# Kernel optimization log

Hardware: AMD Instinct MI355X
Metric: run time of the kernel (lower is better)

Reference implementation:

```python
import jax, jax.numpy as jnp
import numpy as np

N_NODES = 100000
N_EDGES = 3200000
D_FEAT = 64
CLAMP = 20.0
POSINF = 1.0e6
NEGINF = -1.0e6


def setup_inputs() -> dict:
    key = jax.random.key(0)
    k1, k2, k3, k4 = jax.random.split(key, 4)
    x = jax.random.normal(k1, (N_NODES, D_FEAT), dtype=jnp.float32)
    edge_src = jax.random.randint(k2, (N_EDGES,), 0, N_NODES, dtype=jnp.int64 if jax.config.jax_enable_x64 else jnp.int32).astype(jnp.int32)
    edge_dst = jax.random.randint(k3, (N_EDGES,), 0, N_NODES, dtype=jnp.int32)
    # symmetric-normalized-adjacency-like positive weights
    edge_w = jax.random.uniform(k4, (N_EDGES,), dtype=jnp.float32)
    t = jnp.zeros((1,), dtype=jnp.float32)
    return {"t": t, "x": x, "edge_src": edge_src, "edge_dst": edge_dst, "edge_w": edge_w}


def reference(t, x, edge_src, edge_dst, edge_w):
    # out = sparse.mm(G, x): out[dst] += w * x[src]  (COO SpMM via segment_sum)
    msgs = edge_w[:, None] * x[edge_src]                 # [E, d]
    out = jax.ops.segment_sum(msgs, edge_dst, num_segments=N_NODES)  # [N, d]
    # numerical_stability epilogue: nan/inf sanitize + clamp
    out = jnp.nan_to_num(out, nan=0.0, posinf=POSINF, neginf=NEGINF)
    out = jnp.clip(out, -CLAMP, CLAMP)
    return out
```

## Files before the change

### kernel.cpp

```cpp
#include <hip/hip_runtime.h>
#include <hip/hip_fp16.h>
#include <math.h>

#define N_NODES 100000
#define N_EDGES 3200000
#define D_FEAT  64
#define CLAMP_V 20.0f

#define BSH 6
#define BSZ 64
#define NB  1563
#define SBNSH 10
#define NSB 98
#define CPAD 32
#define CHUNKP 4096
#define NCHUNK ((N_EDGES + CHUNKP - 1) / CHUNKP)
#define CAPL 2560
#define HISTB 512
#define NSLC 4
#define NBIN 256
#define GRIDSG 1568
#define CPX (GRIDSG / 8)


__global__ __launch_bounds__(256)
void prep_kernel(const float4* __restrict__ xin, ushort4* __restrict__ xh,
                 const int* __restrict__ edst, int* __restrict__ counts,
                 int n4) {
    __shared__ int h[NSB];
    if (blockIdx.x < HISTB) {
        if (threadIdx.x < NSB) h[threadIdx.x] = 0;
        __syncthreads();
        const int4* d4p = (const int4*)edst;
        int total4 = N_EDGES >> 2;
        for (int i = blockIdx.x * blockDim.x + threadIdx.x; i < total4;
             i += HISTB * blockDim.x) {
            int4 d4 = d4p[i];
            atomicAdd(&h[d4.x >> SBNSH], 1);
            atomicAdd(&h[d4.y >> SBNSH], 1);
            atomicAdd(&h[d4.z >> SBNSH], 1);
            atomicAdd(&h[d4.w >> SBNSH], 1);
        }
        __syncthreads();
        if (threadIdx.x < NSB) {
            int v = h[threadIdx.x];
            if (v) atomicAdd(&counts[threadIdx.x * CPAD], v);
        }
    } else {
        int i = (blockIdx.x - HISTB) * blockDim.x + threadIdx.x;
        if (i < n4) {
            float4 v = xin[i];
            ushort4 o;
            o.x = __half_as_ushort(__float2half(v.x));
            o.y = __half_as_ushort(__float2half(v.y));
            o.z = __half_as_ushort(__float2half(v.z));
            o.w = __half_as_ushort(__float2half(v.w));
            xh[i] = o;
        }
    }
}

__global__ void scan_kernel(const int* __restrict__ counts,
                            int* __restrict__ bstartsSB,
                            int* __restrict__ cursors1) {
    __shared__ int wtot[2];
    int t = threadIdx.x;
    int lane = t & 63, wv = t >> 6;
    int c = (t < NSB) ? counts[t * CPAD] : 0;
    int sc = c;
#pragma unroll
    for (int off = 1; off < 64; off <<= 1) {
        int u = __shfl_up(sc, off);
        if (lane >= off) sc += u;
    }
    if (lane == 63) wtot[wv] = sc;
    __syncthreads();
    int base = (wv == 1) ? wtot[0] : 0;
    int excl = base + sc - c;
    if (t < NSB) {
        bstartsSB[t] = excl;
        cursors1[t * CPAD] = excl;
    }
    if (t == 0) bstartsSB[NSB] = N_EDGES;
}

__global__ __launch_bounds__(512)
void pass1_kernel(const int* __restrict__ esrc,
                  const int* __restrict__ edst,
                  const float* __restrict__ ew,
                  int* __restrict__ cursors1,
                  unsigned* __restrict__ rk32,
                  unsigned short* __restrict__ ra16) {
    __shared__ unsigned       spk[CHUNKP];
    __shared__ unsigned short sax[CHUNKP];
    __shared__ unsigned char  binof[CHUNKP];
    __shared__ int h[NSB];
    __shared__ int hstart[NSB];
    __shared__ int lcur[NSB];
    __shared__ int lbase[NSB];
    __shared__ int wtot[2];

    int c0   = blockIdx.x * CHUNKP;
    int cend = min(c0 + CHUNKP, N_EDGES);
    int n    = cend - c0;
    int nv   = n >> 2;
    const int4*   d4p = (const int4*)(edst + c0);
    const int4*   s4p = (const int4*)(esrc + c0);
    const float4* w4p = (const float4*)(ew + c0);
    int t = threadIdx.x;

    if (t < NSB) h[t] = 0;
    __syncthreads();
    for (int i = t; i < nv; i += 512) {
        int4 d4 = d4p[i];
        atomicAdd(&h[d4.x >> SBNSH], 1);
        atomicAdd(&h[d4.y >> SBNSH], 1);
        atomicAdd(&h[d4.z >> SBNSH], 1);
        atomicAdd(&h[d4.w >> SBNSH], 1);
    }
    __syncthreads();
    int c = 0, sc = 0;
    if (t < 128) {
        c = (t < NSB) ? h[t] : 0;
        sc = c;
#pragma unroll
        for (int off = 1; off < 64; off <<= 1) {
            int u = __shfl_up(sc, off);
            if ((t & 63) >= off) sc += u;
        }
        if ((t & 63) == 63) wtot[t >> 6] = sc;
    }
    __syncthreads();
    if (t < NSB) {
        int base = (t >= 64) ? wtot[0] : 0;
        int excl = base + sc - c;
        hstart[t] = excl;
        lcur[t]   = excl;
        lbase[t]  = c ? atomicAdd(&cursors1[t * CPAD], c) : 0;
    }
    __syncthreads();
    for (int i = t; i < nv; i += 512) {
        int4   d4 = d4p[i];
        int4   s4 = s4p[i];
        float4 w4 = w4p[i];
#define PUT(dd, ss, ww)                                                       \
        {                                                                     \
            int bk  = (dd) >> SBNSH;                                          \
            int pos = atomicAdd(&lcur[bk], 1);                                \
            unsigned hw = __half_as_ushort(__float2half(ww));                 \
            spk[pos] = ((hw & 0xFFFEu) << 16) | (unsigned)(ss);               \
            sax[pos] = (unsigned short)((dd) & 1023);                         \
            binof[pos] = (unsigned char)bk;                                   \
        }
        PUT(d4.x, s4.x, w4.x);
        PUT(d4.y, s4.y, w4.y);
        PUT(d4.z, s4.z, w4.z);
        PUT(d4.w, s4.w, w4.w);
#undef PUT
    }
    __syncthreads();
    for (int i = t; i < n; i += 512) {
        int bk = binof[i];
        int o  = lbase[bk] + (i - hstart[bk]);
        rk32[o] = spk[i];
        ra16[o] = sax[i];
    }
}

__global__ __launch_bounds__(512)
void sort_gather_kernel(const __half* __restrict__ xh,
                        const unsigned* __restrict__ rk32,
                        const unsigned short* __restrict__ ra16,
                        const int* __restrict__ bstartsSB,
                        float* __restrict__ out) {
    __shared__ unsigned      sbuf[CAPL];
    __shared__ unsigned      stg[CAPL];
    __shared__ unsigned char sbin[CAPL];
    __shared__ int h[NBIN + 1];
    __shared__ int cur[NBIN];
    __shared__ int wsum4[4];
    __shared__ int mcnt;
    int t    = threadIdx.x;
    int lane = t & 63;
    int wv   = t >> 6;
    int g    = lane >> 4;
    int s    = lane & 15;
    const char* xbase = (const char*)xh + (s << 3);

    int p = blockIdx.x;
    int b = (p & 7) * CPX + (p >> 3);
    if (b >= NB) return;
    int sbid = b >> 4;
    int fk   = b & 15;
    int sbeg = bstartsSB[sbid];
    int send = bstartsSB[sbid + 1];

    if (t <= NBIN) h[t] = 0;
    if (t == 0) mcnt = 0;
    __syncthreads();
    int a0 = sbeg & ~3;
    for (int i0 = a0 + t * 4; i0 < send; i0 += 512 * 4) {
        int4    r4 = *(const int4*)(rk32 + i0);
        ushort4 a4 = *(const ushort4*)(ra16 + i0);
#define FILT(J, RR, AA)                                                       \
        {                                                                     \
            int idx = i0 + (J);                                               \
            if (idx >= sbeg && idx < send && (int)((AA) >> 6) == fk) {        \
                int bin = (int)((((unsigned)(RR) >> 15) & 3u) << 6)           \
                        | (int)((AA) & 63u);                                  \
                int pos = atomicAdd(&mcnt, 1);                                \
                if (pos < CAPL) {                                             \
                    stg[pos]  = (unsigned)(RR);                               \
                    sbin[pos] = (unsigned char)bin;                           \
                    atomicAdd(&h[bin + 1], 1);                                \
                }                                                             \
            }                                                                 \
        }
        FILT(0, r4.x, a4.x);
        FILT(1, r4.y, a4.y);
        FILT(2, r4.z, a4.z);
        FILT(3, r4.w, a4.w);
#undef FILT
    }
    __syncthreads();
    int cnt = mcnt;
    if (cnt > CAPL) cnt = CAPL;
    if (t < NBIN) {
        int sc = h[t + 1];
#pragma unroll
        for (int off = 1; off < 64; off <<= 1) {
            int u = __shfl_up(sc, off);
            if (lane >= off) sc += u;
        }
        if (lane == 63) wsum4[wv] = sc;
        __syncthreads();
        if (t == 0) {
            int r = 0;
#pragma unroll
            for (int j = 0; j < 4; ++j) { int v = wsum4[j]; wsum4[j] = r; r += v; }
        }
        __syncthreads();
        h[t + 1] = sc + wsum4[wv];
    } else {
        __syncthreads();
        __syncthreads();
    }
    __syncthreads();
    if (t < NBIN) cur[t] = h[t];
    __syncthreads();
    for (int e = t; e < cnt; e += 512) {
        sbuf[atomicAdd(&cur[sbin[e]], 1)] = stg[e];
    }
    __syncthreads();

#define GSTEP(EE, K)                                                         \
    {                                                                        \
        unsigned p2 = sbuf[(EE) + g];                                        \
        float wf = __half2float(__ushort_as_half(                            \
                       (unsigned short)((p2 >> 16) & 0xFFFEu)));             \
        const ushort4 xv = *(const ushort4*)(xbase +                         \
                       ((size_t)((p2 & 0x1FFFFu) << 7)));                    \
        ak0[K] = fmaf(__half2float(__ushort_as_half(xv.x)), wf, ak0[K]);     \
        ak1[K] = fmaf(__half2float(__ushort_as_half(xv.y)), wf, ak1[K]);     \
        ak2[K] = fmaf(__half2float(__ushort_as_half(xv.z)), wf, ak2[K]);     \
        ak3[K] = fmaf(__half2float(__ushort_as_half(xv.w)), wf, ak3[K]);     \
    }
#define GSTEPC(EE, S1, K)                                                    \
    {                                                                        \
        int eg = (EE) + g;                                                   \
        unsigned p2 = sbuf[eg < (S1) ? eg : ((S1) - 1)];                     \
        float wf = (eg < (S1)) ? __half2float(__ushort_as_half(              \
                       (unsigned short)((p2 >> 16) & 0xFFFEu))) : 0.0f;      \
        const ushort4 xv = *(const ushort4*)(xbase +                         \
                       ((size_t)((p2 & 0x1FFFFu) << 7)));                    \
        ak0[K] = fmaf(__half2float(__ushort_as_half(xv.x)), wf, ak0[K]);     \
        ak1[K] = fmaf(__half2float(__ushort_as_half(xv.y)), wf, ak1[K]);     \
        ak2[K] = fmaf(__half2float(__ushort_as_half(xv.z)), wf, ak2[K]);     \
        ak3[K] = fmaf(__half2float(__ushort_as_half(xv.w)), wf, ak3[K]);     \
    }

    int node0 = b << BSH;
    float ak0[8], ak1[8], ak2[8], ak3[8];
#pragma unroll
    for (int k = 0; k < 8; ++k) { ak0[k] = 0.f; ak1[k] = 0.f; ak2[k] = 0.f; ak3[k] = 0.f; }
#pragma unroll 1
    for (int blk = 0; blk < NSLC; ++blk) {
#pragma unroll
        for (int k = 0; k < 8; ++k) {
            int seg = (blk << 6) | ((wv << 3) + k);
            int s0 = h[seg];
            int s1 = h[seg + 1];
            int e = s0;
            for (; e + 8 <= s1; e += 8) {
                GSTEP(e, k);
                GSTEP(e + 4, k);
            }
            for (; e + 4 <= s1; e += 4)
                GSTEP(e, k);
            if (e < s1)
                GSTEPC(e, s1, k);
        }
    }
#pragma unroll
    for (int k = 0; k < 8; ++k) {
        float a0 = ak0[k], a1 = ak1[k], a2 = ak2[k], a3 = ak3[k];
        a0 += __shfl_xor(a0, 16); a0 += __shfl_xor(a0, 32);
        a1 += __shfl_xor(a1, 16); a1 += __shfl_xor(a1, 32);
        a2 += __shfl_xor(a2, 16); a2 += __shfl_xor(a2, 32);
        a3 += __shfl_xor(a3, 16); a3 += __shfl_xor(a3, 32);
        if (isnan(a0)) a0 = 0.0f;
        if (isnan(a1)) a1 = 0.0f;
        if (isnan(a2)) a2 = 0.0f;
        if (isnan(a3)) a3 = 0.0f;
        a0 = fminf(fmaxf(a0, -CLAMP_V), CLAMP_V);
        a1 = fminf(fmaxf(a1, -CLAMP_V), CLAMP_V);
        a2 = fminf(fmaxf(a2, -CLAMP_V), CLAMP_V);
        a3 = fminf(fmaxf(a3, -CLAMP_V), CLAMP_V);
        int node = node0 + (wv << 3) + k;
        if (lane < 16 && node < N_NODES)
            *(float4*)(out + ((size_t)node << 6) + (s << 2)) =
                make_float4(a0, a1, a2, a3);
    }
#undef GSTEP
#undef GSTEPC
}

__global__ void zero_kernel(float4* __restrict__ out, int n4) {
    int i = blockIdx.x * blockDim.x + threadIdx.x;
    if (i < n4) out[i] = make_float4(0.f, 0.f, 0.f, 0.f);
}

__global__ void scatter_kernel(const float* __restrict__ x,
                               const int* __restrict__ esrc,
                               const int* __restrict__ edst,
                               const float* __restrict__ ew,
                               float* __restrict__ out) {
    long long tid = (long long)blockIdx.x * blockDim.x + threadIdx.x;
    int edge = (int)(tid >> 4);
    int q    = (int)(tid & 15);
    if (edge >= N_EDGES) return;
    int   s = esrc[edge];
    int   d = edst[edge];
    float w = ew[edge];
    const float4* xrow = (const float4*)(x + (size_t)s * D_FEAT);
    float4 v = xrow[q];
    float* orow = out + (size_t)d * D_FEAT + q * 4;
    atomicAdd(orow + 0, w * v.x);
    atomicAdd(orow + 1, w * v.y);
    atomicAdd(orow + 2, w * v.z);
    atomicAdd(orow + 3, w * v.w);
}

__global__ void epilogue_kernel(float4* __restrict__ out, int n4) {
    int i = blockIdx.x * blockDim.x + threadIdx.x;
    if (i >= n4) return;
    float4 v = out[i];
    float* p = &v.x;
#pragma unroll
    for (int k = 0; k < 4; ++k) {
        float f = p[k];
        if (isnan(f)) f = 0.0f;
        f = fminf(fmaxf(f, -CLAMP_V), CLAMP_V);
        p[k] = f;
    }
    out[i] = v;
}

extern "C" void kernel_launch(void* const* d_in, const int* in_sizes, int n_in,
                              void* d_out, int out_size, void* d_ws, size_t ws_size,
                              hipStream_t stream) {
    const float* x    = (const float*)d_in[1];
    const int*   esrc = (const int*)d_in[2];
    const int*   edst = (const int*)d_in[3];
    const float* ew   = (const float*)d_in[4];
    float*       out  = (float*)d_out;

    size_t meta_ints = (size_t)NSB * CPAD
                     + (NSB + 1)
                     + (size_t)NSB * CPAD;
    meta_ints = (meta_ints + 3) & ~(size_t)3;
    size_t rk_bytes  = (size_t)N_EDGES * sizeof(unsigned);
    size_t ra_bytes  = (size_t)N_EDGES * sizeof(unsigned short);
    size_t xh_bytes  = (size_t)N_NODES * D_FEAT * sizeof(__half);
    size_t need = meta_ints * sizeof(int) + rk_bytes + ra_bytes + xh_bytes;

    if (ws_size >= need) {
        int*      counts    = (int*)d_ws;
        int*      bstartsSB = counts + (size_t)NSB * CPAD;
        int*      cursors1  = bstartsSB + (NSB + 1);
        unsigned* rk32      = (unsigned*)((int*)d_ws + meta_ints);
        unsigned short* ra16 = (unsigned short*)((char*)rk32 + rk_bytes);
        __half*   xh        = (__half*)((char*)ra16 + ra_bytes);

        hipMemsetAsync(counts, 0, (size_t)NSB * CPAD * sizeof(int), stream);
        {
            int n4 = N_NODES * D_FEAT / 4;
            prep_kernel<<<HISTB + (n4 + 255) / 256, 256, 0, stream>>>(
                (const float4*)x, (ushort4*)xh, edst, counts, n4);
        }
        scan_kernel<<<1, 128, 0, stream>>>(counts, bstartsSB, cursors1);
        pass1_kernel<<<NCHUNK, 512, 0, stream>>>(esrc, edst, ew, cursors1,
                                                 rk32, ra16);
        sort_gather_kernel<<<GRIDSG, 512, 0, stream>>>(xh, rk32, ra16,
                                                       bstartsSB, out);
    } else {
        const int n4 = N_NODES * D_FEAT / 4;
        zero_kernel<<<(n4 + 255) / 256, 256, 0, stream>>>((float4*)out, n4);
        long long total = (long long)N_EDGES * 16;
        scatter_kernel<<<(int)((total + 255) / 256), 256, 0, stream>>>(x, esrc, edst, ew, out);
        epilogue_kernel<<<(n4 + 255) / 256, 256, 0, stream>>>((float4*)out, n4);
    }
}
```

Before: 236.0 us.

## Double gather block to 128 nodes with 1024-thread blocks, halving superblock rescans

Each sort_gather block now owns 128 destination nodes instead of 64 and runs 1024 threads, so each superblock's edge list is filtered by 8 blocks rather than 16. The aim is to halve the redundant reads of rk32/ra16 during the filter phase. The XCD-aware block mapping is rewritten for 782 blocks, and the bin index is rebuilt from the stored key because 512 bins no longer fit in a byte. The cost is larger shared buffers (CAPL 5120), fewer resident blocks per CU, and a higher chance of exceeding capacity on skewed inputs.

```diff
diff --git a/kernel.cpp b/kernel.cpp
--- a/kernel.cpp
+++ b/kernel.cpp
@@ -7,20 +7,18 @@
 #define D_FEAT  64
 #define CLAMP_V 20.0f
 
-#define BSH 6
-#define BSZ 64
-#define NB  1563
+#define BSH 7
+#define BSZ 128
+#define NB  782
 #define SBNSH 10
 #define NSB 98
 #define CPAD 32
 #define CHUNKP 4096
 #define NCHUNK ((N_EDGES + CHUNKP - 1) / CHUNKP)
-#define CAPL 2560
+#define CAPL 5120
 #define HISTB 512
 #define NSLC 4
-#define NBIN 256
-#define GRIDSG 1568
-#define CPX (GRIDSG / 8)
+#define NBIN 512
 
 
 __global__ __launch_bounds__(256)
@@ -167,7 +165,7 @@
     }
 }
 
-__global__ __launch_bounds__(512)
+__global__ __launch_bounds__(1024)
 void sort_gather_kernel(const __half* __restrict__ xh,
                         const unsigned* __restrict__ rk32,
                         const unsigned short* __restrict__ ra16,
@@ -178,7 +176,7 @@
     __shared__ unsigned char sbin[CAPL];
     __shared__ int h[NBIN + 1];
     __shared__ int cur[NBIN];
-    __shared__ int wsum4[4];
+    __shared__ int wsum8[8];
     __shared__ int mcnt;
     int t    = threadIdx.x;
     int lane = t & 63;
@@ -187,11 +185,11 @@
     int s    = lane & 15;
     const char* xbase = (const char*)xh + (s << 3);
 
-    int p = blockIdx.x;
-    int b = (p & 7) * CPX + (p >> 3);
-    if (b >= NB) return;
-    int sbid = b >> 4;
-    int fk   = b & 15;
+    int p   = blockIdx.x;
+    int xcd = p & 7, idx = p >> 3;
+    int b   = ((xcd < 6) ? xcd * 98 : 588 + (xcd - 6) * 97) + idx;
+    int sbid = b >> 3;
+    int fk   = b & 7;
     int sbeg = bstartsSB[sbid];
     int send = bstartsSB[sbid + 1];
 
@@ -199,19 +197,19 @@
     if (t == 0) mcnt = 0;
     __syncthreads();
     int a0 = sbeg & ~3;
-    for (int i0 = a0 + t * 4; i0 < send; i0 += 512 * 4) {
+    for (int i0 = a0 + t * 4; i0 < send; i0 += 1024 * 4) {
         int4    r4 = *(const int4*)(rk32 + i0);
         ushort4 a4 = *(const ushort4*)(ra16 + i0);
 #define FILT(J, RR, AA)                                                       \
         {                                                                     \
-            int idx = i0 + (J);                                               \
-            if (idx >= sbeg && idx < send && (int)((AA) >> 6) == fk) {        \
-                int bin = (int)((((unsigned)(RR) >> 15) & 3u) << 6)           \
-                        | (int)((AA) & 63u);                                  \
+            int idx2 = i0 + (J);                                              \
+            if (idx2 >= sbeg && idx2 < send && (int)((AA) >> 7) == fk) {      \
+                int nd = (int)((AA) & 127u);                                  \
+                int bin = (int)((((unsigned)(RR) >> 15) & 3u) << 7) | nd;     \
                 int pos = atomicAdd(&mcnt, 1);                                \
                 if (pos < CAPL) {                                             \
                     stg[pos]  = (unsigned)(RR);                               \
-                    sbin[pos] = (unsigned char)bin;                           \
+                    sbin[pos] = (unsigned char)nd;                            \
                     atomicAdd(&h[bin + 1], 1);                                \
                 }                                                             \
             }                                                                 \
@@ -225,31 +223,30 @@
     __syncthreads();
     int cnt = mcnt;
     if (cnt > CAPL) cnt = CAPL;
-    if (t < NBIN) {
-        int sc = h[t + 1];
+    {
+        int sc = (t < NBIN) ? h[t + 1] : 0;
 #pragma unroll
         for (int off = 1; off < 64; off <<= 1) {
             int u = __shfl_up(sc, off);
             if (lane >= off) sc += u;
         }
-        if (lane == 63) wsum4[wv] = sc;
+        if (t < NBIN && lane == 63) wsum8[wv] = sc;
         __syncthreads();
         if (t == 0) {
             int r = 0;
 #pragma unroll
-            for (int j = 0; j < 4; ++j) { int v = wsum4[j]; wsum4[j] = r; r += v; }
+            for (int j = 0; j < 8; ++j) { int v = wsum8[j]; wsum8[j] = r; r += v; }
         }
         __syncthreads();
-        h[t + 1] = sc + wsum4[wv];
-    } else {
-        __syncthreads();
-        __syncthreads();
+        if (t < NBIN) h[t + 1] = sc + wsum8[wv];
     }
     __syncthreads();
     if (t < NBIN) cur[t] = h[t];
     __syncthreads();
-    for (int e = t; e < cnt; e += 512) {
-        sbuf[atomicAdd(&cur[sbin[e]], 1)] = stg[e];
+    for (int e = t; e < cnt; e += 1024) {
+        unsigned r = stg[e];
+        int bin = (int)(((r >> 15) & 3u) << 7) | (int)sbin[e];
+        sbuf[atomicAdd(&cur[bin], 1)] = r;
     }
     __syncthreads();
 
@@ -287,7 +284,7 @@
     for (int blk = 0; blk < NSLC; ++blk) {
 #pragma unroll
         for (int k = 0; k < 8; ++k) {
-            int seg = (blk << 6) | ((wv << 3) + k);
+            int seg = (blk << 7) | ((wv << 3) + k);
             int s0 = h[seg];
             int s1 = h[seg + 1];
             int e = s0;
@@ -401,8 +398,8 @@
         scan_kernel<<<1, 128, 0, stream>>>(counts, bstartsSB, cursors1);
         pass1_kernel<<<NCHUNK, 512, 0, stream>>>(esrc, edst, ew, cursors1,
                                                  rk32, ra16);
-        sort_gather_kernel<<<GRIDSG, 512, 0, stream>>>(xh, rk32, ra16,
-                                                       bstartsSB, out);
+        sort_gather_kernel<<<NB, 1024, 0, stream>>>(xh, rk32, ra16,
+                                                    bstartsSB, out);
     } else {
         const int n4 = N_NODES * D_FEAT / 4;
         zero_kernel<<<(n4 + 255) / 256, 256, 0, stream>>>((float4*)out, n4);
```

Result: faster. 227.2 us (-3.7%).
